# Optimization experiments

Measured on AMD Instinct MI355X. Metric: run time of the kernel, lower is better.

The kernel has to match this reference:

```python
import jax, jax.numpy as jnp
import numpy as np

N, IN_DIM, OUT_DIM, HEADS = 50000, 256, 256, 8
C = OUT_DIM // HEADS  # per-head channels = 32
E = 800000
G = 64  # number of graphs in the batch
NEG_SLOPE = 0.2
GN_EPS = 1e-5


def setup_inputs() -> dict:
    key = jax.random.key(0)
    ks = jax.random.split(key, 12)
    x = jax.random.normal(ks[0], (N, IN_DIM), dtype=jnp.float32)
    edge_index = jax.random.randint(ks[1], (2, E), 0, N, dtype=jnp.int64)
    batch = jnp.sort(jax.random.randint(ks[2], (N,), 0, G, dtype=jnp.int64))
    s = 1.0 / np.sqrt(IN_DIM)
    W_l = jax.random.uniform(ks[3], (IN_DIM, HEADS * C), jnp.float32, -s, s)
    b_l = jnp.zeros((HEADS * C,), jnp.float32)
    W_r = jax.random.uniform(ks[4], (IN_DIM, HEADS * C), jnp.float32, -s, s)
    b_r = jnp.zeros((HEADS * C,), jnp.float32)
    att = jax.random.normal(ks[5], (HEADS, C), dtype=jnp.float32) / np.sqrt(C)
    bias = jnp.zeros((HEADS * C,), jnp.float32)
    gn_weight = jnp.ones((OUT_DIM,), jnp.float32)
    gn_bias = jnp.zeros((OUT_DIM,), jnp.float32)
    gn_mean_scale = jnp.ones((OUT_DIM,), jnp.float32)
    return {"x": x, "edge_index": edge_index, "batch": batch,
            "W_l": W_l, "b_l": b_l, "W_r": W_r, "b_r": b_r,
            "att": att, "bias": bias, "gn_weight": gn_weight,
            "gn_bias": gn_bias, "gn_mean_scale": gn_mean_scale}


def _gat_block(x, src, dst, batch, W_l, b_l, W_r, b_r, att, bias,
               gn_weight, gn_bias, gn_mean_scale):
    n = x.shape[0]
    # GATv2Conv (add_self_loops=True, concat=True)
    loops = jnp.arange(n, dtype=src.dtype)
    src = jnp.concatenate([src, loops])
    dst = jnp.concatenate([dst, loops])
    xl = (x @ W_l + b_l).reshape(n, HEADS, C)  # source transform
    xr = (x @ W_r + b_r).reshape(n, HEADS, C)  # target transform
    e = jax.nn.leaky_relu(xl[src] + xr[dst], NEG_SLOPE)  # [E', H, C]
    logits = jnp.einsum('ehc,hc->eh', e, att)            # [E', H]
    # segment softmax over incoming edges of each destination node
    m = jax.ops.segment_max(logits, dst, num_segments=n)
    alpha = jnp.exp(logits - m[dst])
    denom = jax.ops.segment_sum(alpha, dst, num_segments=n)
    alpha = alpha / (denom[dst] + 1e-16)
    msg = xl[src] * alpha[:, :, None]                    # [E', H, C]
    h = jax.ops.segment_sum(msg, dst, num_segments=n).reshape(n, HEADS * C) + bias
    # identity residual (in_dim == out_dim) + ELU
    h = jax.nn.elu(h + x)
    # GraphNorm (post-norm)
    counts = jnp.maximum(jax.ops.segment_sum(jnp.ones((n,), h.dtype), batch,
                                             num_segments=G), 1.0)
    mean = jax.ops.segment_sum(h, batch, num_segments=G) / counts[:, None]
    out0 = h - gn_mean_scale * mean[batch]
    var = jax.ops.segment_sum(out0 * out0, batch, num_segments=G) / counts[:, None]
    return gn_weight * out0 / jnp.sqrt(var[batch] + GN_EPS) + gn_bias


def reference(x, edge_index, batch, W_l, b_l, W_r, b_r, att, bias,
              gn_weight, gn_bias, gn_mean_scale):
    return _gat_block(x, edge_index[0], edge_index[1], batch,
                      W_l, b_l, W_r, b_r, att, bias,
                      gn_weight, gn_bias, gn_mean_scale)
```

## Files before the change

### kernel.cpp

```cpp
#include <hip/hip_runtime.h>
#include <hip/hip_bf16.h>
#include <stdint.h>

#define N_NODES 50000
#define MPAD    50048
#define IN_DIM  256
#define EDGES   800000
#define EPRIME  (EDGES + N_NODES)
#define NGRAPH  64
#define GN_EPS  1e-5f
#define ECPAD   53248
#define NBLK    208

typedef __attribute__((ext_vector_type(8))) short short8;
typedef __attribute__((ext_vector_type(4))) float floatx4;
typedef __attribute__((ext_vector_type(2))) float float2v;

__device__ __forceinline__ uint32_t pk2bf(float a, float b) {
    union { __hip_bfloat162 h; uint32_t u; } cv;
    cv.h = __float22bfloat162_rn(make_float2(a, b));
    return cv.u;
}

__device__ __forceinline__ unsigned short f2b(float f) {
    uint32_t u = __float_as_uint(f);
    u += 0x7fffu + ((u >> 16) & 1u);
    return (unsigned short)(u >> 16);
}

__global__ __launch_bounds__(256) void k_prep_w(const float* __restrict__ Wl,
                                                const float* __restrict__ Wr,
                                                unsigned short* __restrict__ Wt) {
    int idx = blockIdx.x * 256 + threadIdx.x;
    int n = idx >> 8, k = idx & 255;
    float v = (n < 256) ? Wl[k * 256 + n] : Wr[k * 256 + (n - 256)];
    Wt[idx] = f2b(v);
}

__global__ __launch_bounds__(512) void k_gemm(const float* __restrict__ x,
                                              const unsigned short* __restrict__ Wt,
                                              const float* __restrict__ bl,
                                              const float* __restrict__ br,
                                              unsigned short* __restrict__ XL,
                                              unsigned short* __restrict__ XR) {
    __shared__ unsigned short As[64 * 256];
    int rbase = blockIdx.x * 64;
    int tid = threadIdx.x;

#pragma unroll
    for (int it = 0; it < 4; ++it) {
        int c = it * 512 + tid;
        int row = c >> 5, ch = c & 31;
        int gr = rbase + row;
        float4 f0, f1;
        if (gr < N_NODES) {
            const float4* src = (const float4*)(x + (size_t)gr * 256 + ch * 8);
            f0 = src[0]; f1 = src[1];
        } else {
            f0 = make_float4(0.f,0.f,0.f,0.f); f1 = f0;
        }
        uint32_t p0 = pk2bf(f0.x, f0.y), p1 = pk2bf(f0.z, f0.w);
        uint32_t p2 = pk2bf(f1.x, f1.y), p3 = pk2bf(f1.z, f1.w);
        uint4 hv = make_uint4(p0, p1, p2, p3);
        *(uint4*)(As + row * 256 + (ch ^ (row & 7)) * 8) = hv;
    }
    __syncthreads();

    int w = tid >> 6;
    int l = tid & 63;
    int m = l & 15, q = l >> 4;

    floatx4 acc[4][4];
#pragma unroll
    for (int rf = 0; rf < 4; ++rf)
#pragma unroll
        for (int cf = 0; cf < 4; ++cf)
            acc[rf][cf] = (floatx4){0.f, 0.f, 0.f, 0.f};

    const unsigned short* wbase = Wt + (size_t)(w * 64) * 256;

#pragma unroll
    for (int kk = 0; kk < 8; ++kk) {
        short8 a[4];
#pragma unroll
        for (int rf = 0; rf < 4; ++rf) {
            int row = rf * 16 + m;
            int ch = (kk * 4 + q) ^ (row & 7);
            a[rf] = *(const short8*)(As + row * 256 + ch * 8);
        }
#pragma unroll
        for (int cf = 0; cf < 4; ++cf) {
            short8 b = *(const short8*)(wbase + (size_t)(cf * 16 + m) * 256 + kk * 32 + q * 8);
#pragma unroll
            for (int rf = 0; rf < 4; ++rf)
                acc[rf][cf] = __builtin_amdgcn_mfma_f32_16x16x32_bf16(b, a[rf], acc[rf][cf], 0, 0, 0);
        }
    }

    unsigned short* obase = (w < 4) ? XL : XR;
    const float* bptr = (w < 4) ? bl : br;
    int cb = (w & 3) * 64;
#pragma unroll
    for (int cf = 0; cf < 4; ++cf) {
        int chb = cb + cf * 16 + q * 4;
        float4 bv = *(const float4*)(bptr + chb);
#pragma unroll
        for (int rf = 0; rf < 4; ++rf) {
            int node = rbase + rf * 16 + m;
            uint2 o;
            o.x = pk2bf(acc[rf][cf][0] + bv.x, acc[rf][cf][1] + bv.y);
            o.y = pk2bf(acc[rf][cf][2] + bv.z, acc[rf][cf][3] + bv.w);
            *(uint2*)(obase + (size_t)node * 256 + chb) = o;
        }
    }
}

__global__ __launch_bounds__(256) void k_hist(const int* __restrict__ ei,
                                              const int* __restrict__ batch,
                                              int* __restrict__ ecount,
                                              int* __restrict__ ncount,
                                              int* __restrict__ sedge) {
    __shared__ int hist[NGRAPH];
    if (threadIdx.x < NGRAPH) hist[threadIdx.x] = 0;
    __syncthreads();
    int e = blockIdx.x * 256 + threadIdx.x;
    if (e < EPRIME) {
        int d = (e < EDGES) ? ei[EDGES + e] : (e - EDGES);
        atomicAdd(&ecount[d], 1);
    }
    if (e < N_NODES) atomicAdd(&hist[batch[e]], 1);
    if (blockIdx.x == 0 && threadIdx.x < 16) sedge[EPRIME + threadIdx.x] = 0;
    __syncthreads();
    if (threadIdx.x < NGRAPH && hist[threadIdx.x])
        atomicAdd(&ncount[threadIdx.x], hist[threadIdx.x]);
}

__global__ __launch_bounds__(256) void k_scan1(const int* __restrict__ ecount,
                                               int* __restrict__ bsum) {
    __shared__ int red[256];
    int v = ecount[blockIdx.x * 256 + threadIdx.x];
    red[threadIdx.x] = v;
    __syncthreads();
    for (int off = 128; off > 0; off >>= 1) {
        if (threadIdx.x < off) red[threadIdx.x] += red[threadIdx.x + off];
        __syncthreads();
    }
    if (threadIdx.x == 0) bsum[blockIdx.x] = red[0];
}

__global__ __launch_bounds__(256) void k_scan2(int* __restrict__ bsum) {
    __shared__ int buf[256];
    int t = threadIdx.x;
    int v = (t < NBLK) ? bsum[t] : 0;
    buf[t] = v;
    __syncthreads();
    for (int off = 1; off < 256; off <<= 1) {
        int p = (t >= off) ? buf[t - off] : 0;
        __syncthreads();
        buf[t] += p;
        __syncthreads();
    }
    if (t < NBLK) bsum[t] = buf[t] - v;
}

__global__ __launch_bounds__(256) void k_scan3(const int* __restrict__ ecount,
                                               const int* __restrict__ bsum,
                                               int* __restrict__ estart,
                                               int* __restrict__ ecursor) {
    __shared__ int buf[256];
    int b = blockIdx.x, t = threadIdx.x;
    int v = ecount[b * 256 + t];
    buf[t] = v;
    __syncthreads();
    for (int off = 1; off < 256; off <<= 1) {
        int p = (t >= off) ? buf[t - off] : 0;
        __syncthreads();
        buf[t] += p;
        __syncthreads();
    }
    int e = bsum[b] + buf[t] - v;
    estart[b * 256 + t]  = e;
    ecursor[b * 256 + t] = e;
}

__global__ __launch_bounds__(256) void k_scatter(const int* __restrict__ ei,
                                                 int* __restrict__ ecursor,
                                                 int* __restrict__ sedge) {
    int e = blockIdx.x * 256 + threadIdx.x;
    if (e >= EPRIME) return;
    int s, d;
    if (e < EDGES) { s = ei[e]; d = ei[EDGES + e]; }
    else           { s = d = e - EDGES; }
    int pos = atomicAdd(&ecursor[d], 1);
    sedge[pos] = s;
}

__global__ __launch_bounds__(256) void k_msg(const unsigned short* __restrict__ XL,
                                             const unsigned short* __restrict__ XRb,
                                             const float* __restrict__ x,
                                             const float* __restrict__ att,
                                             const float* __restrict__ bias,
                                             const int* __restrict__ sedge,
                                             const int* __restrict__ estart,
                                             const int* __restrict__ ecount,
                                             float* __restrict__ out) {
    int d = (int)((blockIdx.x * 256 + threadIdx.x) >> 6);
    int l = threadIdx.x & 63;
    int lofs = l * 8;

    float4 xin  = ((const float4*)(x + (size_t)d * 256))[l];
    float4 bvv  = ((const float4*)bias)[l];
    float4 attv = ((const float4*)att)[l];
    float2v att01 = {attv.x, attv.y}, att23 = {attv.z, attv.w};

    uint2 xru = ((const uint2*)(XRb + (size_t)d * 256))[l];
    float2v xr01, xr23;
    xr01[0] = __uint_as_float(xru.x << 16);
    xr01[1] = __uint_as_float(xru.x & 0xffff0000u);
    xr23[0] = __uint_as_float(xru.y << 16);
    xr23[1] = __uint_as_float(xru.y & 0xffff0000u);

    int s0  = __builtin_amdgcn_readfirstlane(estart[d]);
    int cnt = __builtin_amdgcn_readfirstlane(ecount[d]);

    auto ldrow = [&](int src) -> uint2 {
        size_t off = ((size_t)(uint32_t)__builtin_amdgcn_readfirstlane(src)) << 9;
        return *(const uint2*)((const char*)XL + off + lofs);
    };

    float den0 = 0.f, den1 = 0.f, den2 = 0.f, den3 = 0.f;
    float2v A01 = {0.f,0.f}, A23 = {0.f,0.f};
    float2v B01 = {0.f,0.f}, B23 = {0.f,0.f};
    float2v C01 = {0.f,0.f}, C23 = {0.f,0.f};
    float2v D01 = {0.f,0.f}, D23 = {0.f,0.f};

    auto proc = [&](uint2 U, float& den, float2v& R01, float2v& R23) {
        float2v x01, x23;
        x01[0] = __uint_as_float(U.x << 16);
        x01[1] = __uint_as_float(U.x & 0xffff0000u);
        x23[0] = __uint_as_float(U.y << 16);
        x23[1] = __uint_as_float(U.y & 0xffff0000u);
        float2v e01 = x01 + xr01, e23 = x23 + xr23;
        float2v f01 = e01 * 0.2f, f23 = e23 * 0.2f;
        e01[0] = fmaxf(e01[0], f01[0]); e01[1] = fmaxf(e01[1], f01[1]);
        e23[0] = fmaxf(e23[0], f23[0]); e23[1] = fmaxf(e23[1], f23[1]);
        float2v pp2 = e01 * att01 + e23 * att23;
        float pp = pp2[0] + pp2[1];
        {
            int pi = __float_as_int(pp);
            pp += __int_as_float(__builtin_amdgcn_update_dpp(0, pi, 0xB1, 0xF, 0xF, true));
            pi = __float_as_int(pp);
            pp += __int_as_float(__builtin_amdgcn_update_dpp(0, pi, 0x4E, 0xF, 0xF, true));
            pp += __int_as_float(__builtin_amdgcn_ds_swizzle(__float_as_int(pp), 0x101F));
        }
        float al = __expf(fminf(pp, 80.f));
        den += al;
        float2v al2 = {al, al};
        R01 += al2 * x01;
        R23 += al2 * x23;
    };

    uint2 P0 = ldrow(sedge[s0]);
    uint2 P1 = ldrow(sedge[s0 + 1]);
    uint2 P2 = ldrow(sedge[s0 + 2]);
    uint2 P3 = ldrow(sedge[s0 + 3]);

    int nq = cnt >> 2;
    for (int qq = 0; qq < nq; ++qq) {
        uint2 Q0 = P0, Q1 = P1, Q2 = P2, Q3 = P3;
        int nb = s0 + (qq + 1) * 4;
        P0 = ldrow(sedge[nb]);
        P1 = ldrow(sedge[nb + 1]);
        P2 = ldrow(sedge[nb + 2]);
        P3 = ldrow(sedge[nb + 3]);
        proc(Q0, den0, A01, A23);
        proc(Q1, den1, B01, B23);
        proc(Q2, den2, C01, C23);
        proc(Q3, den3, D01, D23);
    }
    int rem = cnt & 3;
    if (rem > 0) proc(P0, den0, A01, A23);
    if (rem > 1) proc(P1, den1, B01, B23);
    if (rem > 2) proc(P2, den2, C01, C23);

    float inv = 1.f / ((den0 + den1) + (den2 + den3) + 1e-16f);
    A01 = (A01 + B01) + (C01 + D01);
    A23 = (A23 + B23) + (C23 + D23);

    float h0 = A01[0] * inv + bvv.x + xin.x; h0 = (h0 > 0.f) ? h0 : (__expf(h0) - 1.f);
    float h1 = A01[1] * inv + bvv.y + xin.y; h1 = (h1 > 0.f) ? h1 : (__expf(h1) - 1.f);
    float h2 = A23[0] * inv + bvv.z + xin.z; h2 = (h2 > 0.f) ? h2 : (__expf(h2) - 1.f);
    float h3 = A23[1] * inv + bvv.w + xin.w; h3 = (h3 > 0.f) ? h3 : (__expf(h3) - 1.f);
    ((float4*)(out + (size_t)d * 256))[l] = make_float4(h0, h1, h2, h3);
}

#define GN_ROWS 64
__global__ __launch_bounds__(256) void k_gn_sum(const float* __restrict__ h,
                                                const int* __restrict__ batch,
                                                float* __restrict__ gsum,
                                                float* __restrict__ gsq) {
    __shared__ int bsh[GN_ROWS];
    int r0 = blockIdx.x * GN_ROWS;
    if (threadIdx.x < GN_ROWS) {
        int i = r0 + threadIdx.x;
        bsh[threadIdx.x] = (i < N_NODES) ? batch[i] : -1;
    }
    __syncthreads();
    int c = threadIdx.x;
    float s1 = 0.f, s2 = 0.f;
    int g = bsh[0];
    for (int j = 0; j < GN_ROWS; j += 4) {
        int i = r0 + j;
        if (i >= N_NODES) break;
        bool full = (i + 3 < N_NODES);
        if (full && bsh[j] == g && bsh[j + 3] == g) {
            const float* hp = h + (size_t)i * 256 + c;
            float v0 = hp[0], v1 = hp[256], v2 = hp[512], v3 = hp[768];
            s1 += (v0 + v1) + (v2 + v3);
            s2 += (v0 * v0 + v1 * v1) + (v2 * v2 + v3 * v3);
        } else {
            for (int jj = j; jj < j + 4; ++jj) {
                int ii = r0 + jj;
                if (ii >= N_NODES) break;
                int bg = bsh[jj];
                if (bg != g) {
                    atomicAdd(&gsum[g * 256 + c], s1);
                    atomicAdd(&gsq[g * 256 + c], s2);
                    s1 = 0.f; s2 = 0.f; g = bg;
                }
                float v = h[(size_t)ii * 256 + c];
                s1 += v; s2 += v * v;
            }
        }
    }
    atomicAdd(&gsum[g * 256 + c], s1);
    atomicAdd(&gsq[g * 256 + c], s2);
}

__global__ __launch_bounds__(256) void k_final(float* __restrict__ out,
                                               const int* __restrict__ batch,
                                               const float* __restrict__ gsum,
                                               const float* __restrict__ gsq,
                                               const int* __restrict__ ncount,
                                               const float* __restrict__ gnw,
                                               const float* __restrict__ gnb,
                                               const float* __restrict__ gms) {
    int idx = blockIdx.x * 256 + threadIdx.x;
    int i = idx >> 6, l = idx & 63;
    if (i >= N_NODES) return;
    int g = batch[i];
    float inv = 1.f / fmaxf((float)ncount[g], 1.f);
    float4 hv = ((const float4*)(out + (size_t)i * 256))[l];
    float4 ms = ((const float4*)(gsum + g * 256))[l];
    float4 qs = ((const float4*)(gsq  + g * 256))[l];
    float4 wv = ((const float4*)gnw)[l];
    float4 bv = ((const float4*)gnb)[l];
    float4 sv = ((const float4*)gms)[l];
    float4 o;
    {
        float m = ms.x * inv, q = qs.x * inv;
        o.x = wv.x * (hv.x - sv.x * m) * rsqrtf(q - m * m * sv.x * (2.f - sv.x) + GN_EPS) + bv.x;
    }
    {
        float m = ms.y * inv, q = qs.y * inv;
        o.y = wv.y * (hv.y - sv.y * m) * rsqrtf(q - m * m * sv.y * (2.f - sv.y) + GN_EPS) + bv.y;
    }
    {
        float m = ms.z * inv, q = qs.z * inv;
        o.z = wv.z * (hv.z - sv.z * m) * rsqrtf(q - m * m * sv.z * (2.f - sv.z) + GN_EPS) + bv.z;
    }
    {
        float m = ms.w * inv, q = qs.w * inv;
        o.w = wv.w * (hv.w - sv.w * m) * rsqrtf(q - m * m * sv.w * (2.f - sv.w) + GN_EPS) + bv.w;
    }
    ((float4*)(out + (size_t)i * 256))[l] = o;
}

extern "C" void kernel_launch(void* const* d_in, const int* in_sizes, int n_in,
                              void* d_out, int out_size, void* d_ws, size_t ws_size,
                              hipStream_t stream) {
    const float* x    = (const float*)d_in[0];
    const int*   ei   = (const int*)d_in[1];
    const int*   batch= (const int*)d_in[2];
    const float* Wl   = (const float*)d_in[3];
    const float* bl   = (const float*)d_in[4];
    const float* Wr   = (const float*)d_in[5];
    const float* br   = (const float*)d_in[6];
    const float* att  = (const float*)d_in[7];
    const float* bias = (const float*)d_in[8];
    const float* gnw  = (const float*)d_in[9];
    const float* gnb  = (const float*)d_in[10];
    const float* gms  = (const float*)d_in[11];
    float* out = (float*)d_out;

    char* p = (char*)d_ws;
    auto alloc = [&](size_t bytes) -> char* {
        char* r = p;
        p += (bytes + 255) & ~(size_t)255;
        return r;
    };
    unsigned short* Wt  = (unsigned short*)alloc((size_t)512 * 256 * 2);
    unsigned short* XL  = (unsigned short*)alloc((size_t)MPAD * 256 * 2);
    unsigned short* XRb = (unsigned short*)alloc((size_t)MPAD * 256 * 2);
    int* estart         = (int*)alloc((size_t)ECPAD * 4);
    int* ecursor        = (int*)alloc((size_t)ECPAD * 4);
    int* sedge          = (int*)alloc((size_t)(EPRIME + 16) * 4);
    int* bsum           = (int*)alloc((size_t)256 * 4);
    int* ecount         = (int*)alloc((size_t)ECPAD * 4);
    int* ncount         = (int*)alloc((size_t)NGRAPH * 4);
    float* gsum         = (float*)alloc((size_t)2 * NGRAPH * 256 * 4);
    float* gsq          = gsum + NGRAPH * 256;
    size_t zbytes = (size_t)((char*)(gsum + 2 * NGRAPH * 256) - (char*)ecount);
    hipMemsetAsync(ecount, 0, zbytes, stream);

    k_prep_w<<<512, 256, 0, stream>>>(Wl, Wr, Wt);
    k_gemm<<<MPAD / 64, 512, 0, stream>>>(x, Wt, bl, br, XL, XRb);

    k_hist<<<(EPRIME + 255) / 256, 256, 0, stream>>>(ei, batch, ecount, ncount, sedge);
    k_scan1<<<NBLK, 256, 0, stream>>>(ecount, bsum);
    k_scan2<<<1, 256, 0, stream>>>(bsum);
    k_scan3<<<NBLK, 256, 0, stream>>>(ecount, bsum, estart, ecursor);
    k_scatter<<<(EPRIME + 255) / 256, 256, 0, stream>>>(ei, ecursor, sedge);

    k_msg<<<N_NODES / 4, 256, 0, stream>>>(XL, XRb, x, att, bias,
                                           sedge, estart, ecount, out);

    k_gn_sum<<<(N_NODES + GN_ROWS - 1) / GN_ROWS, 256, 0, stream>>>(out, batch, gsum, gsq);
    k_final<<<N_NODES * 64 / 256, 256, 0, stream>>>(out, batch, gsum, gsq,
                                                    ncount, gnw, gnb, gms);
}
```

Measured before the change: 359.7 us.

## Fuse weight prep with histogram, merge scan passes, hoist GEMM B loads, predicate tail

Merges the weight transpose/convert kernel and the edge/graph histogram kernel into one launch split by block index. It also folds the single-block scan of block sums into the block-sum kernel using an atomic ticket, so the last block does the scan. In the GEMM the B fragments are loaded before the MFMA loop, and the message kernel handles the tail of each edge list with predicated processing instead of branches. The aim is fewer launches and better latency hiding, at the cost of a last-block-done pattern that relies on a ticket counter zeroed by the memset.

```diff
diff --git a/kernel.cpp b/kernel.cpp
--- a/kernel.cpp
+++ b/kernel.cpp
@@ -4,7 +4,6 @@
 
 #define N_NODES 50000
 #define MPAD    50048
-#define IN_DIM  256
 #define EDGES   800000
 #define EPRIME  (EDGES + N_NODES)
 #define NGRAPH  64
@@ -28,13 +27,35 @@
     return (unsigned short)(u >> 16);
 }
 
-__global__ __launch_bounds__(256) void k_prep_w(const float* __restrict__ Wl,
-                                                const float* __restrict__ Wr,
-                                                unsigned short* __restrict__ Wt) {
-    int idx = blockIdx.x * 256 + threadIdx.x;
-    int n = idx >> 8, k = idx & 255;
-    float v = (n < 256) ? Wl[k * 256 + n] : Wr[k * 256 + (n - 256)];
-    Wt[idx] = f2b(v);
+__global__ __launch_bounds__(512) void k_prep(const float* __restrict__ Wl,
+                                              const float* __restrict__ Wr,
+                                              unsigned short* __restrict__ Wt,
+                                              const int* __restrict__ ei,
+                                              const int* __restrict__ batch,
+                                              int* __restrict__ ecount,
+                                              int* __restrict__ ncount,
+                                              int* __restrict__ sedge) {
+    __shared__ int hist[NGRAPH];
+    int b = blockIdx.x;
+    int t = threadIdx.x;
+    if (b < 256) {
+        int idx = b * 512 + t;
+        int n = idx >> 8, k = idx & 255;
+        float v = (n < 256) ? Wl[k * 256 + n] : Wr[k * 256 + (n - 256)];
+        Wt[idx] = f2b(v);
+        return;
+    }
+    if (t < NGRAPH) hist[t] = 0;
+    __syncthreads();
+    int e = (b - 256) * 512 + t;
+    if (e < EPRIME) {
+        int d = (e < EDGES) ? ei[EDGES + e] : (e - EDGES);
+        atomicAdd(&ecount[d], 1);
+    }
+    if (e < N_NODES) atomicAdd(&hist[batch[e]], 1);
+    if (b == 256 && t < 16) sedge[EPRIME + t] = 0;
+    __syncthreads();
+    if (t < NGRAPH && hist[t]) atomicAdd(&ncount[t], hist[t]);
 }
 
 __global__ __launch_bounds__(512) void k_gemm(const float* __restrict__ x,
@@ -59,9 +80,8 @@
         } else {
             f0 = make_float4(0.f,0.f,0.f,0.f); f1 = f0;
         }
-        uint32_t p0 = pk2bf(f0.x, f0.y), p1 = pk2bf(f0.z, f0.w);
-        uint32_t p2 = pk2bf(f1.x, f1.y), p3 = pk2bf(f1.z, f1.w);
-        uint4 hv = make_uint4(p0, p1, p2, p3);
+        uint4 hv = make_uint4(pk2bf(f0.x, f0.y), pk2bf(f0.z, f0.w),
+                              pk2bf(f1.x, f1.y), pk2bf(f1.z, f1.w));
         *(uint4*)(As + row * 256 + (ch ^ (row & 7)) * 8) = hv;
     }
     __syncthreads();
@@ -81,6 +101,10 @@
 
 #pragma unroll
     for (int kk = 0; kk < 8; ++kk) {
+        short8 b[4];
+#pragma unroll
+        for (int cf = 0; cf < 4; ++cf)
+            b[cf] = *(const short8*)(wbase + (size_t)(cf * 16 + m) * 256 + kk * 32 + q * 8);
         short8 a[4];
 #pragma unroll
         for (int rf = 0; rf < 4; ++rf) {
@@ -89,12 +113,10 @@
             a[rf] = *(const short8*)(As + row * 256 + ch * 8);
         }
 #pragma unroll
-        for (int cf = 0; cf < 4; ++cf) {
-            short8 b = *(const short8*)(wbase + (size_t)(cf * 16 + m) * 256 + kk * 32 + q * 8);
+        for (int cf = 0; cf < 4; ++cf)
 #pragma unroll
             for (int rf = 0; rf < 4; ++rf)
-                acc[rf][cf] = __builtin_amdgcn_mfma_f32_16x16x32_bf16(b, a[rf], acc[rf][cf], 0, 0, 0);
-        }
+                acc[rf][cf] = __builtin_amdgcn_mfma_f32_16x16x32_bf16(b[cf], a[rf], acc[rf][cf], 0, 0, 0);
     }
 
     unsigned short* obase = (w < 4) ? XL : XR;
@@ -115,52 +137,38 @@
     }
 }
 
-__global__ __launch_bounds__(256) void k_hist(const int* __restrict__ ei,
-                                              const int* __restrict__ batch,
-                                              int* __restrict__ ecount,
-                                              int* __restrict__ ncount,
-                                              int* __restrict__ sedge) {
-    __shared__ int hist[NGRAPH];
-    if (threadIdx.x < NGRAPH) hist[threadIdx.x] = 0;
-    __syncthreads();
-    int e = blockIdx.x * 256 + threadIdx.x;
-    if (e < EPRIME) {
-        int d = (e < EDGES) ? ei[EDGES + e] : (e - EDGES);
-        atomicAdd(&ecount[d], 1);
-    }
-    if (e < N_NODES) atomicAdd(&hist[batch[e]], 1);
-    if (blockIdx.x == 0 && threadIdx.x < 16) sedge[EPRIME + threadIdx.x] = 0;
-    __syncthreads();
-    if (threadIdx.x < NGRAPH && hist[threadIdx.x])
-        atomicAdd(&ncount[threadIdx.x], hist[threadIdx.x]);
-}
-
 __global__ __launch_bounds__(256) void k_scan1(const int* __restrict__ ecount,
-                                               int* __restrict__ bsum) {
+                                               int* __restrict__ bsum,
+                                               int* __restrict__ ticket) {
     __shared__ int red[256];
-    int v = ecount[blockIdx.x * 256 + threadIdx.x];
-    red[threadIdx.x] = v;
+    __shared__ int buf[256];
+    __shared__ int amlast;
+    int t = threadIdx.x;
+    int v = ecount[blockIdx.x * 256 + t];
+    red[t] = v;
     __syncthreads();
     for (int off = 128; off > 0; off >>= 1) {
-        if (threadIdx.x < off) red[threadIdx.x] += red[threadIdx.x + off];
+        if (t < off) red[t] += red[t + off];
         __syncthreads();
     }
-    if (threadIdx.x == 0) bsum[blockIdx.x] = red[0];
-}
-
-__global__ __launch_bounds__(256) void k_scan2(int* __restrict__ bsum) {
-    __shared__ int buf[256];
-    int t = threadIdx.x;
-    int v = (t < NBLK) ? bsum[t] : 0;
-    buf[t] = v;
-    __syncthreads();
-    for (int off = 1; off < 256; off <<= 1) {
-        int p = (t >= off) ? buf[t - off] : 0;
+    if (t == 0) {
+        __hip_atomic_store(&bsum[blockIdx.x], red[0], __ATOMIC_RELEASE, __HIP_MEMORY_SCOPE_AGENT);
+        int tk = __hip_atomic_fetch_add(ticket, 1, __ATOMIC_ACQ_REL, __HIP_MEMORY_SCOPE_AGENT);
+        amlast = (tk == NBLK - 1);
+    }
+    __syncthreads();
+    if (amlast) {
+        int bv = (t < NBLK) ? __hip_atomic_load(&bsum[t], __ATOMIC_ACQUIRE, __HIP_MEMORY_SCOPE_AGENT) : 0;
+        buf[t] = bv;
         __syncthreads();
-        buf[t] += p;
-        __syncthreads();
-    }
-    if (t < NBLK) bsum[t] = buf[t] - v;
+        for (int off = 1; off < 256; off <<= 1) {
+            int p = (t >= off) ? buf[t - off] : 0;
+            __syncthreads();
+            buf[t] += p;
+            __syncthreads();
+        }
+        if (t < NBLK) bsum[t] = buf[t] - bv;
+    }
 }
 
 __global__ __launch_bounds__(256) void k_scan3(const int* __restrict__ ecount,
@@ -234,54 +242,57 @@
     float2v C01 = {0.f,0.f}, C23 = {0.f,0.f};
     float2v D01 = {0.f,0.f}, D23 = {0.f,0.f};
 
-    auto proc = [&](uint2 U, float& den, float2v& R01, float2v& R23) {
-        float2v x01, x23;
-        x01[0] = __uint_as_float(U.x << 16);
-        x01[1] = __uint_as_float(U.x & 0xffff0000u);
-        x23[0] = __uint_as_float(U.y << 16);
-        x23[1] = __uint_as_float(U.y & 0xffff0000u);
-        float2v e01 = x01 + xr01, e23 = x23 + xr23;
-        float2v f01 = e01 * 0.2f, f23 = e23 * 0.2f;
-        e01[0] = fmaxf(e01[0], f01[0]); e01[1] = fmaxf(e01[1], f01[1]);
-        e23[0] = fmaxf(e23[0], f23[0]); e23[1] = fmaxf(e23[1], f23[1]);
-        float2v pp2 = e01 * att01 + e23 * att23;
-        float pp = pp2[0] + pp2[1];
-        {
-            int pi = __float_as_int(pp);
-            pp += __int_as_float(__builtin_amdgcn_update_dpp(0, pi, 0xB1, 0xF, 0xF, true));
-            pi = __float_as_int(pp);
-            pp += __int_as_float(__builtin_amdgcn_update_dpp(0, pi, 0x4E, 0xF, 0xF, true));
-            pp += __int_as_float(__builtin_amdgcn_ds_swizzle(__float_as_int(pp), 0x101F));
-        }
-        float al = __expf(fminf(pp, 80.f));
-        den += al;
-        float2v al2 = {al, al};
-        R01 += al2 * x01;
-        R23 += al2 * x23;
-    };
+#define PROC(U, VALID, DEN, R01, R23)                                        \
+    {                                                                        \
+        float2v x01, x23;                                                    \
+        x01[0] = __uint_as_float(U.x << 16);                                 \
+        x01[1] = __uint_as_float(U.x & 0xffff0000u);                         \
+        x23[0] = __uint_as_float(U.y << 16);                                 \
+        x23[1] = __uint_as_float(U.y & 0xffff0000u);                         \
+        float2v e01 = x01 + xr01, e23 = x23 + xr23;                          \
+        e01 = __builtin_elementwise_max(e01, e01 * 0.2f);                    \
+        e23 = __builtin_elementwise_max(e23, e23 * 0.2f);                    \
+        float2v pp2 = __builtin_elementwise_fma(e23, att23, e01 * att01);    \
+        float pp = pp2[0] + pp2[1];                                          \
+        int pi = __float_as_int(pp);                                         \
+        pp += __int_as_float(__builtin_amdgcn_update_dpp(0, pi, 0xB1, 0xF, 0xF, true)); \
+        pi = __float_as_int(pp);                                             \
+        pp += __int_as_float(__builtin_amdgcn_update_dpp(0, pi, 0x4E, 0xF, 0xF, true)); \
+        pp += __int_as_float(__builtin_amdgcn_ds_swizzle(__float_as_int(pp), 0x101F)); \
+        float al = __expf(fminf(pp, 80.f));                                  \
+        al = (VALID) ? al : 0.f;                                             \
+        DEN += al;                                                           \
+        float2v al2 = {al, al};                                              \
+        R01 = __builtin_elementwise_fma(al2, x01, R01);                      \
+        R23 = __builtin_elementwise_fma(al2, x23, R23);                      \
+    }
 
     uint2 P0 = ldrow(sedge[s0]);
     uint2 P1 = ldrow(sedge[s0 + 1]);
     uint2 P2 = ldrow(sedge[s0 + 2]);
     uint2 P3 = ldrow(sedge[s0 + 3]);
 
-    int nq = cnt >> 2;
-    for (int qq = 0; qq < nq; ++qq) {
+    int nq = (cnt + 3) >> 2;
+    for (int qq = 0; qq < nq - 1; ++qq) {
         uint2 Q0 = P0, Q1 = P1, Q2 = P2, Q3 = P3;
         int nb = s0 + (qq + 1) * 4;
         P0 = ldrow(sedge[nb]);
         P1 = ldrow(sedge[nb + 1]);
         P2 = ldrow(sedge[nb + 2]);
         P3 = ldrow(sedge[nb + 3]);
-        proc(Q0, den0, A01, A23);
-        proc(Q1, den1, B01, B23);
-        proc(Q2, den2, C01, C23);
-        proc(Q3, den3, D01, D23);
-    }
-    int rem = cnt & 3;
-    if (rem > 0) proc(P0, den0, A01, A23);
-    if (rem > 1) proc(P1, den1, B01, B23);
-    if (rem > 2) proc(P2, den2, C01, C23);
+        PROC(Q0, true, den0, A01, A23);
+        PROC(Q1, true, den1, B01, B23);
+        PROC(Q2, true, den2, C01, C23);
+        PROC(Q3, true, den3, D01, D23);
+    }
+    {
+        int base = (nq - 1) * 4;
+        PROC(P0, base + 0 < cnt, den0, A01, A23);
+        PROC(P1, base + 1 < cnt, den1, B01, B23);
+        PROC(P2, base + 2 < cnt, den2, C01, C23);
+        PROC(P3, base + 3 < cnt, den3, D01, D23);
+    }
+#undef PROC
 
     float inv = 1.f / ((den0 + den1) + (den2 + den3) + 1e-16f);
     A01 = (A01 + B01) + (C01 + D01);
@@ -408,17 +419,17 @@
     int* bsum           = (int*)alloc((size_t)256 * 4);
     int* ecount         = (int*)alloc((size_t)ECPAD * 4);
     int* ncount         = (int*)alloc((size_t)NGRAPH * 4);
+    int* ticket         = (int*)alloc((size_t)64 * 4);
     float* gsum         = (float*)alloc((size_t)2 * NGRAPH * 256 * 4);
     float* gsq          = gsum + NGRAPH * 256;
     size_t zbytes = (size_t)((char*)(gsum + 2 * NGRAPH * 256) - (char*)ecount);
     hipMemsetAsync(ecount, 0, zbytes, stream);
 
-    k_prep_w<<<512, 256, 0, stream>>>(Wl, Wr, Wt);
+    k_prep<<<256 + (EPRIME + 511) / 512, 512, 0, stream>>>(Wl, Wr, Wt, ei, batch,
+                                                           ecount, ncount, sedge);
     k_gemm<<<MPAD / 64, 512, 0, stream>>>(x, Wt, bl, br, XL, XRb);
 
-    k_hist<<<(EPRIME + 255) / 256, 256, 0, stream>>>(ei, batch, ecount, ncount, sedge);
-    k_scan1<<<NBLK, 256, 0, stream>>>(ecount, bsum);
-    k_scan2<<<1, 256, 0, stream>>>(bsum);
+    k_scan1<<<NBLK, 256, 0, stream>>>(ecount, bsum, ticket);
     k_scan3<<<NBLK, 256, 0, stream>>>(ecount, bsum, estart, ecursor);
     k_scatter<<<(EPRIME + 255) / 256, 256, 0, stream>>>(ei, ecursor, sedge);
 
```

Result: no change. 366.6 us (+1.9%).
